# Kernel optimization log

Hardware: AMD Instinct MI355X
Metric: run time of the kernel (lower is better)

## Reference

```python
import jax, jax.numpy as jnp
import numpy as np

TOKEN_DIM = 768
HIDDEN_DIM = 384
PATCH_SCALE = 2
SELECTED_RATIO = 0.15


def setup_inputs() -> dict:
    key = jax.random.key(0)
    ks = jax.random.split(key, 12)
    B, T, D = 32, 1024, TOKEN_DIM
    Thr = T * PATCH_SCALE * PATCH_SCALE  # 4096
    flat_dim = D * PATCH_SCALE * PATCH_SCALE  # 3072
    H = HIDDEN_DIM
    s = lambda fan_in: 1.0 / np.sqrt(fan_in)
    inp = {
        "base_tokens": jax.random.normal(ks[0], (B, T, D), jnp.float32),
        "highres_tokens": jax.random.normal(ks[1], (B, Thr, D), jnp.float32),
        "selection_scores": jax.random.normal(ks[2], (B, T), jnp.float32),
        # local_refine: Linear(flat_dim,H) -> GELU -> Linear(H,D)
        "W1": jax.random.uniform(ks[3], (flat_dim, H), jnp.float32, -s(flat_dim), s(flat_dim)),
        "b1": jax.random.uniform(ks[4], (H,), jnp.float32, -s(flat_dim), s(flat_dim)),
        "W2": jax.random.uniform(ks[5], (H, D), jnp.float32, -s(H), s(H)),
        "b2": jax.random.uniform(ks[6], (D,), jnp.float32, -s(H), s(H)),
        # blend_gate: Linear(2D+1,H) -> SiLU -> Linear(H,1)
        "Wg1": jax.random.uniform(ks[7], (2 * D + 1, H), jnp.float32, -s(2 * D + 1), s(2 * D + 1)),
        "bg1": jax.random.uniform(ks[8], (H,), jnp.float32, -s(2 * D + 1), s(2 * D + 1)),
        "Wg2": jax.random.uniform(ks[9], (H, 1), jnp.float32, -s(H), s(H)),
        "bg2": jax.random.uniform(ks[10], (1,), jnp.float32, -s(H), s(H)),
    }
    return inp


def reference(base_tokens, highres_tokens, selection_scores,
              W1, b1, W2, b2, Wg1, bg1, Wg2, bg2):
    B, T, D = base_tokens.shape
    S = PATCH_SCALE
    g = int(round(np.sqrt(T)))  # coarse grid side
    # strided patch reshape: [B, g, S, g, S, D] -> [B, g, g, S, S, D] -> [B, T, S*S*D]
    local = highres_tokens.reshape(B, g, S, g, S, D)
    local = local.transpose(0, 1, 3, 2, 4, 5).reshape(B, T, S * S * D)
    # local refine MLP (exact-erf GELU matches torch nn.GELU default)
    h = jax.nn.gelu(jnp.einsum('btf,fh->bth', local, W1) + b1, approximate=False)
    refined_local = jnp.einsum('bth,hd->btd', h, W2) + b2
    # blend gate
    gate_in = jnp.concatenate([base_tokens, refined_local, selection_scores[..., None]], axis=-1)
    hg = jax.nn.silu(jnp.einsum('btf,fh->bth', gate_in, Wg1) + bg1)
    gate = jax.nn.sigmoid(jnp.einsum('bth,ho->bto', hg, Wg2) + bg2)  # [B, T, 1]
    # top-k selection mask (static k)
    topk = max(1, int(round(T * SELECTED_RATIO)))
    topk_idx = jax.lax.top_k(selection_scores, topk)[1]  # [B, k]
    mask = jnp.zeros((B, T), base_tokens.dtype).at[jnp.arange(B)[:, None], topk_idx].set(1.0)
    refined = base_tokens + mask[..., None] * gate * (refined_local - base_tokens)
    return refined
```

## Files before the change

kernel.cpp:

```cpp
#include <hip/hip_runtime.h>
#include <cstdint>

#define NB    32
#define NTOK  1024
#define D_    768
#define NHR   4096
#define HID   384
#define KSEL  154
#define MSEL  4928
#define MT_   77
#define FLAT  3072

typedef short  s16x8 __attribute__((ext_vector_type(8)));
typedef unsigned short u16x8 __attribute__((ext_vector_type(8)));
typedef unsigned short u16x4 __attribute__((ext_vector_type(4)));
typedef float  f32x4 __attribute__((ext_vector_type(4)));

__device__ inline unsigned short f2bf(float f) {
    uint32_t u = __builtin_bit_cast(uint32_t, f);
    u += 0x7FFFu + ((u >> 16) & 1u);
    return (unsigned short)(u >> 16);
}
__device__ inline float bf2f(unsigned short h) {
    uint32_t u = ((uint32_t)h) << 16;
    return __builtin_bit_cast(float, u);
}
__device__ inline s16x8 cvt8(const float* __restrict__ p) {
    float4 v0 = *(const float4*)p, v1 = *(const float4*)(p + 4);
    s16x8 r;
    r[0]=(short)f2bf(v0.x); r[1]=(short)f2bf(v0.y); r[2]=(short)f2bf(v0.z); r[3]=(short)f2bf(v0.w);
    r[4]=(short)f2bf(v1.x); r[5]=(short)f2bf(v1.y); r[6]=(short)f2bf(v1.z); r[7]=(short)f2bf(v1.w);
    return r;
}

#define OFF_SEL   0
#define OFF_RMAP  32768
#define OFF_GPART 163840
#define OFF_W1T   401408
#define OFF_W2T   2760704
#define OFF_WG1T  3350528
#define OFF_H     4530176
#define OFF_RL    8314880
#define DOUT_P0   0
#define DOUT_P1   (MSEL * HID * 4)

__global__ __launch_bounds__(1024) void prep_kernel(
    const float* __restrict__ scores, int* __restrict__ sel, int* __restrict__ rmap,
    const float* __restrict__ W1, const float* __restrict__ W2, const float* __restrict__ Wg1,
    unsigned short* __restrict__ W1t, unsigned short* __restrict__ W2t,
    unsigned short* __restrict__ Wg1t)
{
    __shared__ float s[NTOK];
    __shared__ int cnt;
    __shared__ unsigned short T[4][64][66];
    const int bid = blockIdx.x;
    if (bid < NB) {
        const int b = bid;
        const int t = threadIdx.x;
        s[t] = scores[b * NTOK + t];
        if (t == 0) cnt = 0;
        __syncthreads();
        float v = s[t];
        int rank = 0;
        for (int j = 0; j < NTOK; ++j) {
            float vj = s[j];
            rank += (vj > v) || (vj == v && j < t);
        }
        int rm = -1;
        if (rank < KSEL) {
            int pos = atomicAdd(&cnt, 1);
            rm = b * KSEL + pos;
            sel[rm] = t;
        }
        rmap[b * NTOK + t] = rm;
    } else {
        const int g = threadIdx.x >> 8;
        const int tid = threadIdx.x & 255;
        const int tile = (bid - NB) * 4 + g;
        const float* src; unsigned short* dst; int K, N, kt, nt;
        if (tile < 288)      { src = W1;  dst = W1t;  K = FLAT; N = HID; nt = tile % 6;  kt = tile / 6;  }
        else if (tile < 360) { int l = tile - 288; src = W2;  dst = W2t;  K = HID;  N = D_;  nt = l % 12; kt = l / 12; }
        else                 { int l = tile - 360; src = Wg1; dst = Wg1t; K = 1536; N = HID; nt = l % 6;  kt = l / 6;  }
        const int k0 = kt * 64, n0 = nt * 64;
        {
            const int ln = tid & 63, kc = tid >> 6;
            #pragma unroll
            for (int j = 0; j < 16; ++j)
                T[g][ln][kc * 16 + j] = f2bf(src[(uint64_t)(k0 + kc * 16 + j) * N + n0 + ln]);
        }
        __syncthreads();
        {
            const int row = tid >> 2, c0 = (tid & 3) * 16;
            u16x8 v0, v1;
            #pragma unroll
            for (int p = 0; p < 8; ++p) { v0[p] = T[g][row][c0 + p]; v1[p] = T[g][row][c0 + 8 + p]; }
            *(u16x8*)(dst + (uint64_t)(n0 + row) * K + k0 + c0) = v0;
            *(u16x8*)(dst + (uint64_t)(n0 + row) * K + k0 + c0 + 8) = v1;
        }
    }
}

template <int MODE>
__global__ __launch_bounds__(256) void gemm_mfma(
    const float* __restrict__ Araw,
    const unsigned short* __restrict__ Abf,
    const unsigned short* __restrict__ Bt,
    const float* __restrict__ bias,
    const int* __restrict__ sel,
    const float* __restrict__ scores,
    const float* __restrict__ WgLast,
    const float* __restrict__ Wg2,
    void* __restrict__ Cout,
    float* __restrict__ Pout,
    float* __restrict__ gpart)
{
    constexpr int K = MODE == 0 ? FLAT : (MODE == 1 ? HID : 2 * D_);
    constexpr int N = MODE == 1 ? D_ : HID;
    constexpr int NT = N / 64;
    constexpr int KLEN = (MODE == 0) ? 1536 : K;
    constexpr int NSTEP = KLEN / 64;

    const int lin = blockIdx.x;
    const int xcd = lin & 7;
    int j = lin >> 3;
    const int ntile = j % NT; j /= NT;
    const int mhi = j % 10;
    const int split = j / 10;
    const int mt = mhi * 8 + xcd;
    if (mt >= MT_) return;
    const int m0 = mt * 64;
    const int n0 = ntile * 64;
    const int kb = split * 1536;
    float* P = (MODE == 0) ? (Pout + (uint64_t)split * MSEL * HID) : nullptr;

    __shared__ unsigned short As[2][64 * 64];
    __shared__ unsigned short Bs[2][64 * 64];
    __shared__ uint32_t offT[64 * 4];
    __shared__ float scv[64];

    const int tid = threadIdx.x;
    const int lane = tid & 63;
    const int wid = tid >> 6;
    const int wm = wid >> 1;
    const int wn = wid & 1;

    if (tid < 64) {
        int r = m0 + tid;
        if (MODE == 0) {
            int b = r / KSEL, t = sel[r];
            int gy = t >> 5, gx = t & 31;
            #pragma unroll
            for (int p = 0; p < 4; ++p) {
                int hr = (gy * 2 + (p >> 1)) * 64 + gx * 2 + (p & 1);
                offT[tid * 4 + p] = (uint32_t)(b * NHR + hr) * D_;
            }
        } else if (MODE == 2) {
            int b = r / KSEL, t = sel[r];
            offT[tid * 4] = (uint32_t)(b * NTOK + t) * D_;
            scv[tid] = scores[b * NTOK + t];
        }
    }
    if (MODE != 1) __syncthreads();

    const int sr0 = tid >> 3;
    const int sc0 = tid & 7;

    auto loadA = [&](int k0, int half, s16x8& dst) {
        int r = sr0 + half * 32;
        int k = k0 + sc0 * 8;
        if (MODE == 0) {
            int p = k / D_;
            int col = k - p * D_;
            dst = cvt8(Araw + offT[r * 4 + p] + col);
        } else if (MODE == 1) {
            dst = *(const s16x8*)(Abf + (uint64_t)(m0 + r) * HID + k);
        } else {
            if (k < D_) dst = cvt8(Araw + offT[r * 4] + k);
            else        dst = *(const s16x8*)(Abf + (uint64_t)(m0 + r) * D_ + (k - D_));
        }
    };
    auto loadB = [&](int k0, int half, s16x8& dst) {
        int r = sr0 + half * 32;
        dst = *(const s16x8*)(Bt + (uint64_t)(n0 + r) * K + k0 + sc0 * 8);
    };
    auto writeTile = [&](int buf, s16x8* a, s16x8* b) {
        #pragma unroll
        for (int half = 0; half < 2; ++half) {
            int r = sr0 + half * 32;
            int c = sc0 ^ (r & 7);
            *(s16x8*)&As[buf][r * 64 + c * 8] = a[half];
            *(s16x8*)&Bs[buf][r * 64 + c * 8] = b[half];
        }
    };

    f32x4 acc[2][2];
    #pragma unroll
    for (int i = 0; i < 2; ++i)
        #pragma unroll
        for (int jj = 0; jj < 2; ++jj) acc[i][jj] = (f32x4){0.f, 0.f, 0.f, 0.f};

    s16x8 aR[2], bR[2];
    loadA(kb, 0, aR[0]); loadA(kb, 1, aR[1]);
    loadB(kb, 0, bR[0]); loadB(kb, 1, bR[1]);
    writeTile(0, aR, bR);
    __syncthreads();
    if (NSTEP > 1) {
        loadA(kb + 64, 0, aR[0]); loadA(kb + 64, 1, aR[1]);
        loadB(kb + 64, 0, bR[0]); loadB(kb + 64, 1, bR[1]);
    }

    int cur = 0;
    for (int t = 0; t < NSTEP; ++t) {
        #pragma unroll
        for (int kk = 0; kk < 2; ++kk) {
            s16x8 af[2], bfr[2];
            #pragma unroll
            for (int i = 0; i < 2; ++i) {
                int row  = wm * 32 + i * 16 + (lane & 15);
                int cch  = (kk * 4 + (lane >> 4)) ^ (row & 7);
                af[i] = *(const s16x8*)&As[cur][row * 64 + cch * 8];
                int nrow = wn * 32 + i * 16 + (lane & 15);
                int cchb = (kk * 4 + (lane >> 4)) ^ (nrow & 7);
                bfr[i] = *(const s16x8*)&Bs[cur][nrow * 64 + cchb * 8];
            }
            #pragma unroll
            for (int i = 0; i < 2; ++i)
                #pragma unroll
                for (int jj = 0; jj < 2; ++jj)
                    acc[i][jj] = __builtin_amdgcn_mfma_f32_16x16x32_bf16(af[i], bfr[jj], acc[i][jj], 0, 0, 0);
        }
        if (t + 1 < NSTEP) {
            writeTile(cur ^ 1, aR, bR);
            __syncthreads();
            if (t + 2 < NSTEP) {
                int k0 = kb + (t + 2) * 64;
                loadA(k0, 0, aR[0]); loadA(k0, 1, aR[1]);
                loadB(k0, 0, bR[0]); loadB(k0, 1, bR[1]);
            }
            cur ^= 1;
        }
    }

    if (MODE == 2) {
        float wg2v[2] = { Wg2[n0 + wn * 32 + (lane & 15)],
                          Wg2[n0 + wn * 32 + 16 + (lane & 15)] };
        float psum[2][4];
        #pragma unroll
        for (int i = 0; i < 2; ++i)
            #pragma unroll
            for (int reg = 0; reg < 4; ++reg) psum[i][reg] = 0.f;
        #pragma unroll
        for (int i = 0; i < 2; ++i) {
            #pragma unroll
            for (int jj = 0; jj < 2; ++jj) {
                #pragma unroll
                for (int reg = 0; reg < 4; ++reg) {
                    int m = m0 + wm * 32 + i * 16 + (lane >> 4) * 4 + reg;
                    int n = n0 + wn * 32 + jj * 16 + (lane & 15);
                    float x = acc[i][jj][reg] + bias[n] + scv[m - m0] * WgLast[n];
                    x = x / (1.0f + __expf(-x));
                    psum[i][reg] += x * wg2v[jj];
                }
            }
        }
        #pragma unroll
        for (int mask = 1; mask < 16; mask <<= 1)
            #pragma unroll
            for (int i = 0; i < 2; ++i)
                #pragma unroll
                for (int reg = 0; reg < 4; ++reg)
                    psum[i][reg] += __shfl_xor(psum[i][reg], mask);
        if ((lane & 15) == 0) {
            #pragma unroll
            for (int i = 0; i < 2; ++i)
                #pragma unroll
                for (int reg = 0; reg < 4; ++reg) {
                    int m = m0 + wm * 32 + i * 16 + (lane >> 4) * 4 + reg;
                    gpart[m * 12 + ntile * 2 + wn] = psum[i][reg];
                }
        }
        return;
    }
    #pragma unroll
    for (int i = 0; i < 2; ++i) {
        #pragma unroll
        for (int jj = 0; jj < 2; ++jj) {
            #pragma unroll
            for (int reg = 0; reg < 4; ++reg) {
                int m = m0 + wm * 32 + i * 16 + (lane >> 4) * 4 + reg;
                int n = n0 + wn * 32 + jj * 16 + (lane & 15);
                if (MODE == 0) {
                    P[(uint64_t)m * HID + n] = acc[i][jj][reg];
                } else {
                    float x = acc[i][jj][reg] + bias[n];
                    ((unsigned short*)Cout)[(uint64_t)m * D_ + n] = f2bf(x);
                }
            }
        }
    }
}

__global__ __launch_bounds__(256) void combine_kernel(
    const float* __restrict__ P0, const float* __restrict__ P1,
    const float* __restrict__ b1, unsigned short* __restrict__ h)
{
    const int idx = (blockIdx.x * 256 + threadIdx.x) * 8;
    const int col = idx % HID;
    float4 a0 = *(const float4*)(P0 + idx), a1 = *(const float4*)(P0 + idx + 4);
    float4 c0 = *(const float4*)(P1 + idx), c1 = *(const float4*)(P1 + idx + 4);
    float4 bb0 = *(const float4*)(b1 + col), bb1 = *(const float4*)(b1 + col + 4);
    float xs[8] = { a0.x + c0.x + bb0.x, a0.y + c0.y + bb0.y,
                    a0.z + c0.z + bb0.z, a0.w + c0.w + bb0.w,
                    a1.x + c1.x + bb1.x, a1.y + c1.y + bb1.y,
                    a1.z + c1.z + bb1.z, a1.w + c1.w + bb1.w };
    u16x8 v;
    #pragma unroll
    for (int p = 0; p < 8; ++p) {
        float x = xs[p];
        x = 0.5f * x * (1.0f + erff(x * 0.70710678118654752f));
        v[p] = f2bf(x);
    }
    *(u16x8*)(h + idx) = v;
}

__global__ __launch_bounds__(256) void finalize_kernel(
    const int* __restrict__ rmap,
    const float* __restrict__ gpart, const float* __restrict__ bg2,
    const float* __restrict__ base, const unsigned short* __restrict__ rl,
    float* __restrict__ out)
{
    const int lane = threadIdx.x & 63;
    const int row = blockIdx.x * 4 + (threadIdx.x >> 6);
    const int rm = rmap[row];

    const uint64_t bo = (uint64_t)row * D_;
    const float4* b4 = (const float4*)(base + bo);
    float4* o4 = (float4*)(out + bo);

    if (rm < 0) {
        #pragma unroll
        for (int i = 0; i < 3; ++i) o4[lane + 64 * i] = b4[lane + 64 * i];
        return;
    }
    const float4* gp = (const float4*)(gpart + (uint64_t)rm * 12);
    float4 g0 = gp[0], g1 = gp[1], g2 = gp[2];
    float sum = g0.x + g0.y + g0.z + g0.w + g1.x + g1.y + g1.z + g1.w
              + g2.x + g2.y + g2.z + g2.w + bg2[0];
    float gate = 1.0f / (1.0f + __expf(-sum));

    const u16x4* r4 = (const u16x4*)(rl + (uint64_t)rm * D_);
    #pragma unroll
    for (int i = 0; i < 3; ++i) {
        int idx = lane + 64 * i;
        float4 bb = b4[idx];
        u16x4 rr = r4[idx];
        float4 oo;
        oo.x = bb.x + gate * (bf2f(rr[0]) - bb.x);
        oo.y = bb.y + gate * (bf2f(rr[1]) - bb.y);
        oo.z = bb.z + gate * (bf2f(rr[2]) - bb.z);
        oo.w = bb.w + gate * (bf2f(rr[3]) - bb.w);
        o4[idx] = oo;
    }
}

extern "C" void kernel_launch(void* const* d_in, const int* in_sizes, int n_in,
                              void* d_out, int out_size, void* d_ws, size_t ws_size,
                              hipStream_t stream) {
    const float* base   = (const float*)d_in[0];
    const float* hires  = (const float*)d_in[1];
    const float* scores = (const float*)d_in[2];
    const float* W1  = (const float*)d_in[3];
    const float* b1  = (const float*)d_in[4];
    const float* W2  = (const float*)d_in[5];
    const float* b2  = (const float*)d_in[6];
    const float* Wg1 = (const float*)d_in[7];
    const float* bg1 = (const float*)d_in[8];
    const float* Wg2 = (const float*)d_in[9];
    const float* bg2 = (const float*)d_in[10];
    float* out = (float*)d_out;

    char* ws = (char*)d_ws;
    int*            sel   = (int*)(ws + OFF_SEL);
    int*            rmap  = (int*)(ws + OFF_RMAP);
    float*          gpart = (float*)(ws + OFF_GPART);
    unsigned short* W1t   = (unsigned short*)(ws + OFF_W1T);
    unsigned short* W2t   = (unsigned short*)(ws + OFF_W2T);
    unsigned short* Wg1t  = (unsigned short*)(ws + OFF_WG1T);
    unsigned short* h     = (unsigned short*)(ws + OFF_H);
    unsigned short* rl    = (unsigned short*)(ws + OFF_RL);
    float*          P0    = (float*)((char*)d_out + DOUT_P0);
    float*          P1    = (float*)((char*)d_out + DOUT_P1);

    prep_kernel<<<dim3(NB + 126), dim3(1024), 0, stream>>>(scores, sel, rmap,
                                                           W1, W2, Wg1, W1t, W2t, Wg1t);
    gemm_mfma<0><<<dim3(8 * 10 * 6 * 2), dim3(256), 0, stream>>>(
        hires, nullptr, W1t, nullptr, sel, nullptr, nullptr, nullptr, nullptr, P0, nullptr);
    combine_kernel<<<dim3(924), dim3(256), 0, stream>>>(P0, P1, b1, h);
    gemm_mfma<1><<<dim3(8 * 10 * 12), dim3(256), 0, stream>>>(
        nullptr, h, W2t, b2, nullptr, nullptr, nullptr, nullptr, rl, nullptr, nullptr);
    gemm_mfma<2><<<dim3(8 * 10 * 6), dim3(256), 0, stream>>>(
        base, rl, Wg1t, bg1, sel, scores, Wg1 + (uint64_t)1536 * HID, Wg2,
        nullptr, nullptr, gpart);
    finalize_kernel<<<dim3(NB * NTOK / 4), dim3(256), 0, stream>>>(rmap, gpart, bg2, base, rl, out);
}
```

Baseline: 157.9 us.

## Pre-gather patches to bf16 and fuse split-K reduction with GELU via atomic flags

A separate gather kernel converts the selected high-res patches into a contiguous bf16 A matrix, so the first GEMM reads dense bf16 rows instead of doing strided fp32 gathers with conversion inside the K-loop. The split-K combine kernel is removed. The last of the two split blocks to finish a tile, detected with an atomic counter, sums both partials, adds bias, applies GELU and writes h. This trades one launch and the in-loop conversion for an extra gather pass through memory, plus threadfence and atomic overhead and a flag buffer reset in prep.

```diff
diff --git a/kernel.cpp b/kernel.cpp
--- a/kernel.cpp
+++ b/kernel.cpp
@@ -36,19 +36,20 @@
 #define OFF_SEL   0
 #define OFF_RMAP  32768
 #define OFF_GPART 163840
-#define OFF_W1T   401408
-#define OFF_W2T   2760704
-#define OFF_WG1T  3350528
-#define OFF_H     4530176
-#define OFF_RL    8314880
-#define DOUT_P0   0
-#define DOUT_P1   (MSEL * HID * 4)
+#define OFF_FLAG  400384
+#define OFF_W1T   402432
+#define OFF_W2T   2761728
+#define OFF_WG1T  3351552
+#define OFF_H     4531200
+#define OFF_RL    8315904
+#define DOUT_P0   32505856
+#define DOUT_P1   (DOUT_P0 + MSEL * HID * 4)
 
 __global__ __launch_bounds__(1024) void prep_kernel(
     const float* __restrict__ scores, int* __restrict__ sel, int* __restrict__ rmap,
     const float* __restrict__ W1, const float* __restrict__ W2, const float* __restrict__ Wg1,
     unsigned short* __restrict__ W1t, unsigned short* __restrict__ W2t,
-    unsigned short* __restrict__ Wg1t)
+    unsigned short* __restrict__ Wg1t, int* __restrict__ flags)
 {
     __shared__ float s[NTOK];
     __shared__ int cnt;
@@ -57,6 +58,7 @@
     if (bid < NB) {
         const int b = bid;
         const int t = threadIdx.x;
+        if (b == 0 && t < MT_ * 6) flags[t] = 0;
         s[t] = scores[b * NTOK + t];
         if (t == 0) cnt = 0;
         __syncthreads();
@@ -100,6 +102,23 @@
     }
 }
 
+__global__ __launch_bounds__(256) void gather_kernel(
+    const int* __restrict__ sel, const float* __restrict__ highres,
+    unsigned short* __restrict__ Aloc) {
+    const int r = blockIdx.x;
+    const int b = r / KSEL;
+    const int t = sel[r];
+    const int gy = t >> 5, gx = t & 31;
+    for (int ch = threadIdx.x; ch < 384; ch += 256) {
+        int k8 = ch * 8;
+        int p = k8 / D_;
+        int col = k8 - p * D_;
+        int hr = (gy * 2 + (p >> 1)) * 64 + gx * 2 + (p & 1);
+        s16x8 v = cvt8(highres + ((uint64_t)b * NHR + hr) * D_ + col);
+        *(s16x8*)(Aloc + (uint64_t)r * FLAT + k8) = v;
+    }
+}
+
 template <int MODE>
 __global__ __launch_bounds__(256) void gemm_mfma(
     const float* __restrict__ Araw,
@@ -112,7 +131,8 @@
     const float* __restrict__ Wg2,
     void* __restrict__ Cout,
     float* __restrict__ Pout,
-    float* __restrict__ gpart)
+    float* __restrict__ gpart,
+    int* __restrict__ flags)
 {
     constexpr int K = MODE == 0 ? FLAT : (MODE == 1 ? HID : 2 * D_);
     constexpr int N = MODE == 1 ? D_ : HID;
@@ -130,13 +150,13 @@
     if (mt >= MT_) return;
     const int m0 = mt * 64;
     const int n0 = ntile * 64;
-    const int kb = split * 1536;
-    float* P = (MODE == 0) ? (Pout + (uint64_t)split * MSEL * HID) : nullptr;
+    const int kb = (MODE == 0) ? split * 1536 : 0;
 
     __shared__ unsigned short As[2][64 * 64];
     __shared__ unsigned short Bs[2][64 * 64];
-    __shared__ uint32_t offT[64 * 4];
+    __shared__ uint32_t offT[64];
     __shared__ float scv[64];
+    __shared__ int who;
 
     const int tid = threadIdx.x;
     const int lane = tid & 63;
@@ -144,23 +164,14 @@
     const int wm = wid >> 1;
     const int wn = wid & 1;
 
-    if (tid < 64) {
-        int r = m0 + tid;
-        if (MODE == 0) {
-            int b = r / KSEL, t = sel[r];
-            int gy = t >> 5, gx = t & 31;
-            #pragma unroll
-            for (int p = 0; p < 4; ++p) {
-                int hr = (gy * 2 + (p >> 1)) * 64 + gx * 2 + (p & 1);
-                offT[tid * 4 + p] = (uint32_t)(b * NHR + hr) * D_;
-            }
-        } else if (MODE == 2) {
-            int b = r / KSEL, t = sel[r];
-            offT[tid * 4] = (uint32_t)(b * NTOK + t) * D_;
+    if (MODE == 2) {
+        if (tid < 64) {
+            int r = m0 + tid, b = r / KSEL, t = sel[r];
+            offT[tid] = (uint32_t)(b * NTOK + t) * D_;
             scv[tid] = scores[b * NTOK + t];
         }
-    }
-    if (MODE != 1) __syncthreads();
+        __syncthreads();
+    }
 
     const int sr0 = tid >> 3;
     const int sc0 = tid & 7;
@@ -169,13 +180,11 @@
         int r = sr0 + half * 32;
         int k = k0 + sc0 * 8;
         if (MODE == 0) {
-            int p = k / D_;
-            int col = k - p * D_;
-            dst = cvt8(Araw + offT[r * 4 + p] + col);
+            dst = *(const s16x8*)(Abf + (uint64_t)(m0 + r) * FLAT + k);
         } else if (MODE == 1) {
             dst = *(const s16x8*)(Abf + (uint64_t)(m0 + r) * HID + k);
         } else {
-            if (k < D_) dst = cvt8(Araw + offT[r * 4] + k);
+            if (k < D_) dst = cvt8(Araw + offT[r] + k);
             else        dst = *(const s16x8*)(Abf + (uint64_t)(m0 + r) * D_ + (k - D_));
         }
     };
@@ -241,6 +250,45 @@
         }
     }
 
+    if (MODE == 0) {
+        float* P = Pout + (uint64_t)split * (MSEL * HID);
+        #pragma unroll
+        for (int i = 0; i < 2; ++i)
+            #pragma unroll
+            for (int jj = 0; jj < 2; ++jj)
+                #pragma unroll
+                for (int reg = 0; reg < 4; ++reg) {
+                    int m = m0 + wm * 32 + i * 16 + (lane >> 4) * 4 + reg;
+                    int n = n0 + wn * 32 + jj * 16 + (lane & 15);
+                    P[(uint64_t)m * HID + n] = acc[i][jj][reg];
+                }
+        __threadfence();
+        __syncthreads();
+        if (tid == 0) who = atomicAdd(&flags[mt * 6 + ntile], 1);
+        __syncthreads();
+        if (who == 1) {
+            __threadfence();
+            const float* Pa = Pout;
+            const float* Pb = Pout + MSEL * HID;
+            const int r = tid >> 2;
+            const int c0 = (tid & 3) * 16;
+            const uint64_t o = (uint64_t)(m0 + r) * HID + (n0 + c0);
+            unsigned short* H = (unsigned short*)Cout;
+            #pragma unroll
+            for (int hseg = 0; hseg < 2; ++hseg) {
+                u16x8 v;
+                #pragma unroll
+                for (int p = 0; p < 8; ++p) {
+                    float x = Pa[o + hseg * 8 + p] + Pb[o + hseg * 8 + p]
+                            + bias[n0 + c0 + hseg * 8 + p];
+                    x = 0.5f * x * (1.0f + erff(x * 0.70710678118654752f));
+                    v[p] = f2bf(x);
+                }
+                *(u16x8*)(H + o + hseg * 8) = v;
+            }
+        }
+        return;
+    }
     if (MODE == 2) {
         float wg2v[2] = { Wg2[n0 + wn * 32 + (lane & 15)],
                           Wg2[n0 + wn * 32 + 16 + (lane & 15)] };
@@ -282,45 +330,16 @@
         return;
     }
     #pragma unroll
-    for (int i = 0; i < 2; ++i) {
-        #pragma unroll
-        for (int jj = 0; jj < 2; ++jj) {
+    for (int i = 0; i < 2; ++i)
+        #pragma unroll
+        for (int jj = 0; jj < 2; ++jj)
             #pragma unroll
             for (int reg = 0; reg < 4; ++reg) {
                 int m = m0 + wm * 32 + i * 16 + (lane >> 4) * 4 + reg;
                 int n = n0 + wn * 32 + jj * 16 + (lane & 15);
-                if (MODE == 0) {
-                    P[(uint64_t)m * HID + n] = acc[i][jj][reg];
-                } else {
-                    float x = acc[i][jj][reg] + bias[n];
-                    ((unsigned short*)Cout)[(uint64_t)m * D_ + n] = f2bf(x);
-                }
+                float x = acc[i][jj][reg] + bias[n];
+                ((unsigned short*)Cout)[(uint64_t)m * D_ + n] = f2bf(x);
             }
-        }
-    }
-}
-
-__global__ __launch_bounds__(256) void combine_kernel(
-    const float* __restrict__ P0, const float* __restrict__ P1,
-    const float* __restrict__ b1, unsigned short* __restrict__ h)
-{
-    const int idx = (blockIdx.x * 256 + threadIdx.x) * 8;
-    const int col = idx % HID;
-    float4 a0 = *(const float4*)(P0 + idx), a1 = *(const float4*)(P0 + idx + 4);
-    float4 c0 = *(const float4*)(P1 + idx), c1 = *(const float4*)(P1 + idx + 4);
-    float4 bb0 = *(const float4*)(b1 + col), bb1 = *(const float4*)(b1 + col + 4);
-    float xs[8] = { a0.x + c0.x + bb0.x, a0.y + c0.y + bb0.y,
-                    a0.z + c0.z + bb0.z, a0.w + c0.w + bb0.w,
-                    a1.x + c1.x + bb1.x, a1.y + c1.y + bb1.y,
-                    a1.z + c1.z + bb1.z, a1.w + c1.w + bb1.w };
-    u16x8 v;
-    #pragma unroll
-    for (int p = 0; p < 8; ++p) {
-        float x = xs[p];
-        x = 0.5f * x * (1.0f + erff(x * 0.70710678118654752f));
-        v[p] = f2bf(x);
-    }
-    *(u16x8*)(h + idx) = v;
 }
 
 __global__ __launch_bounds__(256) void finalize_kernel(
@@ -383,23 +402,24 @@
     int*            sel   = (int*)(ws + OFF_SEL);
     int*            rmap  = (int*)(ws + OFF_RMAP);
     float*          gpart = (float*)(ws + OFF_GPART);
+    int*            flags = (int*)(ws + OFF_FLAG);
     unsigned short* W1t   = (unsigned short*)(ws + OFF_W1T);
     unsigned short* W2t   = (unsigned short*)(ws + OFF_W2T);
     unsigned short* Wg1t  = (unsigned short*)(ws + OFF_WG1T);
     unsigned short* h     = (unsigned short*)(ws + OFF_H);
     unsigned short* rl    = (unsigned short*)(ws + OFF_RL);
+    unsigned short* Aloc  = (unsigned short*)d_out;
     float*          P0    = (float*)((char*)d_out + DOUT_P0);
-    float*          P1    = (float*)((char*)d_out + DOUT_P1);
 
     prep_kernel<<<dim3(NB + 126), dim3(1024), 0, stream>>>(scores, sel, rmap,
-                                                           W1, W2, Wg1, W1t, W2t, Wg1t);
+                                                           W1, W2, Wg1, W1t, W2t, Wg1t, flags);
+    gather_kernel<<<dim3(MSEL), dim3(256), 0, stream>>>(sel, hires, Aloc);
     gemm_mfma<0><<<dim3(8 * 10 * 6 * 2), dim3(256), 0, stream>>>(
-        hires, nullptr, W1t, nullptr, sel, nullptr, nullptr, nullptr, nullptr, P0, nullptr);
-    combine_kernel<<<dim3(924), dim3(256), 0, stream>>>(P0, P1, b1, h);
+        nullptr, Aloc, W1t, b1, nullptr, nullptr, nullptr, nullptr, h, P0, nullptr, flags);
     gemm_mfma<1><<<dim3(8 * 10 * 12), dim3(256), 0, stream>>>(
-        nullptr, h, W2t, b2, nullptr, nullptr, nullptr, nullptr, rl, nullptr, nullptr);
+        nullptr, h, W2t, b2, nullptr, nullptr, nullptr, nullptr, rl, nullptr, nullptr, nullptr);
     gemm_mfma<2><<<dim3(8 * 10 * 6), dim3(256), 0, stream>>>(
         base, rl, Wg1t, bg1, sel, scores, Wg1 + (uint64_t)1536 * HID, Wg2,
-        nullptr, nullptr, gpart);
+        nullptr, nullptr, gpart, nullptr);
     finalize_kernel<<<dim3(NB * NTOK / 4), dim3(256), 0, stream>>>(rmap, gpart, bg2, base, rl, out);
 }
```

Result: slower. 328.1 us (+107.8%).
